# Performance work log

Measured on AMD Instinct MI355X. Metric: run time of the kernel, lower is better.

The kernel has to match this reference:

```python
import jax, jax.numpy as jnp
import numpy as np

N = 10000   # num nodes
E = 640000  # num edges
D_IN, D_HID, D_OUT = 128, 256, 128


def _cheb_layer(x, src, dst, dis, W0, W1, b):
    """PyG ChebConv with K=2, sym norm, lambda_max=2.0 (no edge weights):
    out = x @ W0 + (L_hat x) @ W1 + b, with L_hat = -D^{-1/2} A D^{-1/2}."""
    norm = -(dis[src] * dis[dst])                       # [E]
    msg = norm[:, None] * x[src]                        # [E, d]
    tx1 = jax.ops.segment_sum(msg, dst, num_segments=N)  # [N, d]
    return x @ W0 + tx1 @ W1 + b


def setup_inputs() -> dict:
    key = jax.random.key(0)
    ks = jax.random.split(key, 10)

    def glorot(k, fan_in, fan_out):
        s = jnp.sqrt(6.0 / (fan_in + fan_out))
        return jax.random.uniform(k, (fan_in, fan_out), jnp.float32, -s, s)

    x = jax.random.normal(ks[0], (N, D_IN), jnp.float32)
    edge_index = jax.random.randint(ks[1], (2, E), 0, N, jnp.int64)
    edge_type = jax.random.randint(ks[2], (E,), 0, 5, jnp.int64)
    return {
        "x": x,
        "edge_index": edge_index,
        "edge_type": edge_type,
        "W01": glorot(ks[3], D_IN, D_HID),
        "W11": glorot(ks[4], D_IN, D_HID),
        "b1": jnp.zeros((D_HID,), jnp.float32),
        "W02": glorot(ks[5], D_HID, D_HID),
        "W12": glorot(ks[6], D_HID, D_HID),
        "b2": jnp.zeros((D_HID,), jnp.float32),
        "W03": glorot(ks[7], D_HID, D_OUT),
        "W13": glorot(ks[8], D_HID, D_OUT),
        "b3": jnp.zeros((D_OUT,), jnp.float32),
    }


def reference(x, edge_index, edge_type, W01, W11, b1, W02, W12, b2, W03, W13, b3):
    # edge_type is unused by ChebConv (matches the original forward signature).
    src, dst = edge_index[0], edge_index[1]
    deg = jax.ops.segment_sum(jnp.ones((E,), x.dtype), src, num_segments=N)
    dis = jnp.where(deg > 0, jax.lax.rsqrt(jnp.maximum(deg, 1.0)), 0.0)
    # eval mode: dropout(p=0.4) is identity
    h = jax.nn.relu(_cheb_layer(x, src, dst, dis, W01, W11, b1))
    h = jax.nn.relu(_cheb_layer(h, src, dst, dis, W02, W12, b2))
    return _cheb_layer(h, src, dst, dis, W03, W13, b3)
```

## Files before the change

### kernel.cpp

```cpp
#include <hip/hip_runtime.h>

#define D_IN 128
#define D_HID 256
#define D_OUT 128
#define NBIN 10240
#define HB 128

typedef __attribute__((ext_vector_type(8))) unsigned short ushort8v;
typedef __attribute__((ext_vector_type(4))) unsigned short ushort4v;
typedef __attribute__((ext_vector_type(8))) short short8v;
typedef __attribute__((ext_vector_type(4))) float f32x4;

__device__ __forceinline__ unsigned short f2bf(float f) {
    unsigned u = __float_as_uint(f);
    unsigned r = (u + 0x7fffu + ((u >> 16) & 1u)) >> 16;
    return (unsigned short)r;
}
__device__ __forceinline__ float bf2f(unsigned short b) {
    return __uint_as_float((unsigned)b << 16);
}


__global__ __launch_bounds__(256) void k_hist(const int* __restrict__ src, const int* __restrict__ dst,
                                              unsigned short* __restrict__ psrc,
                                              unsigned short* __restrict__ pdst,
                                              int E, int EPB) {
    __shared__ int hs[NBIN];
    __shared__ int hd[NBIN];
    int b = blockIdx.x, t = threadIdx.x;
    for (int i = t; i < NBIN; i += 256) { hs[i] = 0; hd[i] = 0; }
    __syncthreads();
    int beg = b * EPB, end = beg + EPB; if (end > E) end = E;
    for (int e = beg + t; e < end; e += 256) {
        atomicAdd(&hs[src[e]], 1);
        atomicAdd(&hd[dst[e]], 1);
    }
    __syncthreads();
    for (int i = t; i < NBIN; i += 256) {
        psrc[(size_t)b * NBIN + i] = (unsigned short)hs[i];
        pdst[(size_t)b * NBIN + i] = (unsigned short)hd[i];
    }
}


__global__ __launch_bounds__(256) void k_colsum(const unsigned short* __restrict__ psrc,
                                                unsigned short* __restrict__ pdst,
                                                float* __restrict__ dis, int* __restrict__ cnt) {
    int bin = blockIdx.x * 256 + threadIdx.x;
    if (bin >= NBIN) return;
    int degs = 0;
    for (int b = 0; b < HB; ++b) degs += psrc[(size_t)b * NBIN + bin];
    int c = 0;
    for (int b = 0; b < HB; ++b) {
        int v = pdst[(size_t)b * NBIN + bin];
        pdst[(size_t)b * NBIN + bin] = (unsigned short)c;
        c += v;
    }
    dis[bin] = degs > 0 ? rsqrtf((float)degs) : 0.f;
    cnt[bin] = c;
}


__global__ void k_scan(const int* __restrict__ cnt, int* __restrict__ off, int n, int E) {
    __shared__ int sums[256];
    int t = threadIdx.x;
    int chunk = (n + 255) / 256;
    int beg = t * chunk;
    int end = beg + chunk; if (end > n) end = n;
    int s = 0;
    for (int i = beg; i < end; ++i) s += cnt[i];
    sums[t] = s;
    __syncthreads();
    if (t == 0) {
        int running = 0;
        for (int i = 0; i < 256; ++i) { int tmp = sums[i]; sums[i] = running; running += tmp; }
        off[n] = E;
    }
    __syncthreads();
    int pre = sums[t];
    for (int i = beg; i < end; ++i) { off[i] = pre; pre += cnt[i]; }
}


__global__ __launch_bounds__(256) void k_scatter2(const int* __restrict__ src, const int* __restrict__ dst,
                                                  const float* __restrict__ dis, const int* __restrict__ off,
                                                  const unsigned short* __restrict__ pfx,
                                                  int2* __restrict__ edges, int E, int EPB) {
    __shared__ int lcnt[NBIN];
    int b = blockIdx.x, t = threadIdx.x;
    for (int i = t; i < NBIN; i += 256) lcnt[i] = 0;
    __syncthreads();
    int beg = b * EPB, end = beg + EPB; if (end > E) end = E;
    const unsigned short* pf = pfx + (size_t)b * NBIN;
    for (int e = beg + t; e < end; e += 256) {
        int s = src[e], d = dst[e];
        int r = atomicAdd(&lcnt[d], 1);
        int pos = off[d] + (int)pf[d] + r;
        float nv = -(dis[s] * dis[d]);
        edges[pos] = make_int2(s, __float_as_int(nv));
    }
}


struct WtrArgs {
    const float* W[6];
    unsigned short* T[6];
    int K[6];
    int N[6];
    const float* xin;
    unsigned short* xout;
    int nElem;
};

__global__ __launch_bounds__(256) void k_wtr7(WtrArgs args) {
    __shared__ float tile[32][33];
    int z = blockIdx.z;
    if (z == 6) {
        int bid = blockIdx.y * 8 + blockIdx.x;
        int stride = 64 * 256 * 4;
        for (int i = (bid * 256 + threadIdx.x) * 4; i < args.nElem; i += stride) {
            float4 v = *reinterpret_cast<const float4*>(&args.xin[i]);
            ushort4v o;
            o[0] = f2bf(v.x); o[1] = f2bf(v.y); o[2] = f2bf(v.z); o[3] = f2bf(v.w);
            *reinterpret_cast<ushort4v*>(&args.xout[i]) = o;
        }
        return;
    }
    const float* W = args.W[z];
    unsigned short* Wt = args.T[z];
    int K = args.K[z], N = args.N[z];
    int k0 = blockIdx.x * 32, n0 = blockIdx.y * 32;
    if (k0 >= K || n0 >= N) return;
    int tx = threadIdx.x & 31, ty = threadIdx.x >> 5;
    for (int i = ty; i < 32; i += 8) tile[i][tx] = W[(size_t)(k0 + i) * N + n0 + tx];
    __syncthreads();
    for (int i = ty; i < 32; i += 8) Wt[(size_t)(n0 + i) * K + k0 + tx] = f2bf(tile[tx][i]);
}


template<int D, bool STBF, bool STF32, bool ADDB>
__global__ __launch_bounds__(256) void k_agg_bf(const int* __restrict__ off,
                                                const int2* __restrict__ edges,
                                                const unsigned short* __restrict__ xb,
                                                unsigned short* __restrict__ outb,
                                                float* __restrict__ outf,
                                                const float* __restrict__ base, int n) {
    const int CHUNK = 128;
    const int TPN = CHUNK / 8;
    const int NPB = 256 / TPN;
    int tid = threadIdx.x;
    int node = blockIdx.x * NPB + tid / TPN;
    if (node >= n) return;
    int cbase = blockIdx.y * CHUNK + (tid % TPN) * 8;
    int i = off[node], end = off[node + 1];
    float acc[8] = {};
    for (; i + 7 < end; i += 8) {
        int2 e[8];
        #pragma unroll
        for (int u = 0; u < 8; ++u) e[u] = edges[i + u];
        ushort8v v[8];
        #pragma unroll
        for (int u = 0; u < 8; ++u)
            v[u] = *reinterpret_cast<const ushort8v*>(&xb[(size_t)e[u].x * D + cbase]);
        #pragma unroll
        for (int u = 0; u < 8; ++u) {
            float nv = __int_as_float(e[u].y);
            #pragma unroll
            for (int j = 0; j < 8; ++j)
                acc[j] += nv * bf2f(v[u][j]);
        }
    }
    for (; i + 1 < end; i += 2) {
        int2 e0 = edges[i], e1 = edges[i + 1];
        ushort8v v0 = *reinterpret_cast<const ushort8v*>(&xb[(size_t)e0.x * D + cbase]);
        ushort8v v1 = *reinterpret_cast<const ushort8v*>(&xb[(size_t)e1.x * D + cbase]);
        float n0 = __int_as_float(e0.y), n1 = __int_as_float(e1.y);
        #pragma unroll
        for (int j = 0; j < 8; ++j)
            acc[j] += n0 * bf2f(v0[j]) + n1 * bf2f(v1[j]);
    }
    if (i < end) {
        int2 e0 = edges[i];
        float n0 = __int_as_float(e0.y);
        ushort8v v0 = *reinterpret_cast<const ushort8v*>(&xb[(size_t)e0.x * D + cbase]);
        #pragma unroll
        for (int j = 0; j < 8; ++j)
            acc[j] += n0 * bf2f(v0[j]);
    }
    if (ADDB) {
        float4 b0 = *reinterpret_cast<const float4*>(&base[(size_t)node * D + cbase]);
        float4 b1 = *reinterpret_cast<const float4*>(&base[(size_t)node * D + cbase + 4]);
        acc[0] += b0.x; acc[1] += b0.y; acc[2] += b0.z; acc[3] += b0.w;
        acc[4] += b1.x; acc[5] += b1.y; acc[6] += b1.z; acc[7] += b1.w;
    }
    if (STBF) {
        ushort8v ob;
        #pragma unroll
        for (int j = 0; j < 8; ++j) ob[j] = f2bf(acc[j]);
        *reinterpret_cast<ushort8v*>(&outb[(size_t)node * D + cbase]) = ob;
    }
    if (STF32) {
        float4 o0, o1;
        o0.x = acc[0]; o0.y = acc[1]; o0.z = acc[2]; o0.w = acc[3];
        o1.x = acc[4]; o1.y = acc[5]; o1.z = acc[6]; o1.w = acc[7];
        *reinterpret_cast<float4*>(&outf[(size_t)node * D + cbase]) = o0;
        *reinterpret_cast<float4*>(&outf[(size_t)node * D + cbase + 4]) = o1;
    }
}


#define LDT 72

template<int K, bool RELU, bool HAS_B2, bool HAS_BIAS, bool ST_BF, bool ST_F32>
__global__ __launch_bounds__(256) void k_gemm_mfma(
        const unsigned short* __restrict__ A1, const unsigned short* __restrict__ W0t,
        const unsigned short* __restrict__ A2, const unsigned short* __restrict__ W1t,
        const float* __restrict__ bias,
        float* __restrict__ C, unsigned short* __restrict__ Cb, int M, int N) {
    __shared__ unsigned short As[64 * LDT];
    __shared__ unsigned short Bs[128 * LDT];
    int tid = threadIdx.x, lane = tid & 63, wave = tid >> 6;
    int wm = wave >> 1, wn = wave & 1;
    int row0 = blockIdx.x * 64, col0 = blockIdx.y * 128;
    f32x4 acc[2][4];
    #pragma unroll
    for (int i = 0; i < 2; ++i)
        #pragma unroll
        for (int j = 0; j < 4; ++j)
            acc[i][j] = (f32x4){0.f, 0.f, 0.f, 0.f};

    int aRow = wm * 32 + (lane & 15);
    int bRow = wn * 64 + (lane & 15);
    int kOff = (lane >> 4) * 8;
    int sr = tid >> 2, sc = (tid & 3) * 8;
    int gra = row0 + sr; if (gra >= M) gra = M - 1;

    const int npass = HAS_B2 ? 2 : 1;
    for (int pass = 0; pass < npass; ++pass) {
        const unsigned short* A = pass ? A2 : A1;
        const unsigned short* W = pass ? W1t : W0t;
        for (int k0 = 0; k0 < K; k0 += 64) {
            #pragma unroll
            for (int h = 0; h < 2; ++h) {
                ushort8v va = *reinterpret_cast<const ushort8v*>(&A[(size_t)gra * K + k0 + sc + h * 32]);
                *reinterpret_cast<ushort8v*>(&As[sr * LDT + sc + h * 32]) = va;
            }
            #pragma unroll
            for (int g = 0; g < 2; ++g)
                #pragma unroll
                for (int h = 0; h < 2; ++h) {
                    int r = sr + g * 64;
                    ushort8v vb = *reinterpret_cast<const ushort8v*>(&W[(size_t)(col0 + r) * K + k0 + sc + h * 32]);
                    *reinterpret_cast<ushort8v*>(&Bs[r * LDT + sc + h * 32]) = vb;
                }
            __syncthreads();
            #pragma unroll
            for (int kk = 0; kk < 2; ++kk) {
                int ko = kOff + kk * 32;
                short8v a[2], bb[4];
                #pragma unroll
                for (int i = 0; i < 2; ++i)
                    a[i] = *reinterpret_cast<const short8v*>(&As[(aRow + i * 16) * LDT + ko]);
                #pragma unroll
                for (int i = 0; i < 4; ++i)
                    bb[i] = *reinterpret_cast<const short8v*>(&Bs[(bRow + i * 16) * LDT + ko]);
                #pragma unroll
                for (int mi = 0; mi < 2; ++mi)
                    #pragma unroll
                    for (int ni = 0; ni < 4; ++ni)
                        acc[mi][ni] = __builtin_amdgcn_mfma_f32_16x16x32_bf16(a[mi], bb[ni], acc[mi][ni], 0, 0, 0);
            }
            __syncthreads();
        }
    }

    int colBase = col0 + wn * 64 + (lane & 15);
    int rowSub = (lane >> 4) * 4;
    #pragma unroll
    for (int mi = 0; mi < 2; ++mi) {
        int rowF = row0 + wm * 32 + mi * 16 + rowSub;
        #pragma unroll
        for (int r = 0; r < 4; ++r) {
            int gr = rowF + r;
            if (gr < M) {
                #pragma unroll
                for (int ni = 0; ni < 4; ++ni) {
                    int gc = colBase + ni * 16;
                    float v = acc[mi][ni][r];
                    if (HAS_BIAS) v += bias[gc];
                    if (RELU)     v = fmaxf(v, 0.f);
                    if (ST_F32)   C[(size_t)gr * N + gc] = v;
                    if (ST_BF)    Cb[(size_t)gr * N + gc] = f2bf(v);
                }
            }
        }
    }
}


template<int K>
__global__ __launch_bounds__(256) void k_gemm_dual(
        const unsigned short* __restrict__ A1, const unsigned short* __restrict__ W03t,
        const unsigned short* __restrict__ W13t, const float* __restrict__ bias,
        float* __restrict__ part, unsigned short* __restrict__ y3b, int M) {
    const int N = 128;
    __shared__ unsigned short As[64 * LDT];
    __shared__ unsigned short Bs[128 * LDT];
    int tid = threadIdx.x, lane = tid & 63, wave = tid >> 6;
    int wm = wave >> 1, wn = wave & 1;
    int row0 = blockIdx.x * 64;
    const unsigned short* W = blockIdx.y ? W13t : W03t;
    f32x4 acc[2][4];
    #pragma unroll
    for (int i = 0; i < 2; ++i)
        #pragma unroll
        for (int j = 0; j < 4; ++j)
            acc[i][j] = (f32x4){0.f, 0.f, 0.f, 0.f};

    int aRow = wm * 32 + (lane & 15);
    int bRow = wn * 64 + (lane & 15);
    int kOff = (lane >> 4) * 8;
    int sr = tid >> 2, sc = (tid & 3) * 8;
    int gra = row0 + sr; if (gra >= M) gra = M - 1;

    for (int k0 = 0; k0 < K; k0 += 64) {
        #pragma unroll
        for (int h = 0; h < 2; ++h) {
            ushort8v va = *reinterpret_cast<const ushort8v*>(&A1[(size_t)gra * K + k0 + sc + h * 32]);
            *reinterpret_cast<ushort8v*>(&As[sr * LDT + sc + h * 32]) = va;
        }
        #pragma unroll
        for (int g = 0; g < 2; ++g)
            #pragma unroll
            for (int h = 0; h < 2; ++h) {
                int r = sr + g * 64;
                ushort8v vb = *reinterpret_cast<const ushort8v*>(&W[(size_t)r * K + k0 + sc + h * 32]);
                *reinterpret_cast<ushort8v*>(&Bs[r * LDT + sc + h * 32]) = vb;
            }
        __syncthreads();
        #pragma unroll
        for (int kk = 0; kk < 2; ++kk) {
            int ko = kOff + kk * 32;
            short8v a[2], bb[4];
            #pragma unroll
            for (int i = 0; i < 2; ++i)
                a[i] = *reinterpret_cast<const short8v*>(&As[(aRow + i * 16) * LDT + ko]);
            #pragma unroll
            for (int i = 0; i < 4; ++i)
                bb[i] = *reinterpret_cast<const short8v*>(&Bs[(bRow + i * 16) * LDT + ko]);
            #pragma unroll
            for (int mi = 0; mi < 2; ++mi)
                #pragma unroll
                for (int ni = 0; ni < 4; ++ni)
                    acc[mi][ni] = __builtin_amdgcn_mfma_f32_16x16x32_bf16(a[mi], bb[ni], acc[mi][ni], 0, 0, 0);
        }
        __syncthreads();
    }

    int colBase = wn * 64 + (lane & 15);
    int rowSub = (lane >> 4) * 4;
    bool isPart = (blockIdx.y == 0);
    #pragma unroll
    for (int mi = 0; mi < 2; ++mi) {
        int rowF = row0 + wm * 32 + mi * 16 + rowSub;
        #pragma unroll
        for (int r = 0; r < 4; ++r) {
            int gr = rowF + r;
            if (gr < M) {
                #pragma unroll
                for (int ni = 0; ni < 4; ++ni) {
                    int gc = colBase + ni * 16;
                    float v = acc[mi][ni][r];
                    if (isPart) part[(size_t)gr * N + gc] = v + bias[gc];
                    else        y3b[(size_t)gr * N + gc] = f2bf(v);
                }
            }
        }
    }
}


extern "C" void kernel_launch(void* const* d_in, const int* in_sizes, int n_in,
                              void* d_out, int out_size, void* d_ws, size_t ws_size,
                              hipStream_t stream) {
    const float* x   = (const float*)d_in[0];
    const int*   ei  = (const int*)d_in[1];
    const float* W01 = (const float*)d_in[3];
    const float* W11 = (const float*)d_in[4];
    const float* b1  = (const float*)d_in[5];
    const float* W02 = (const float*)d_in[6];
    const float* W12 = (const float*)d_in[7];
    const float* b2  = (const float*)d_in[8];
    const float* W03 = (const float*)d_in[9];
    const float* W13 = (const float*)d_in[10];
    const float* b3  = (const float*)d_in[11];
    float* out = (float*)d_out;

    const int n = in_sizes[0] / D_IN;
    const int E = in_sizes[1] / 2;
    const int* src = ei;
    const int* dst = ei + E;
    const int EPB = (E + HB - 1) / HB;

    char* wsb = (char*)d_ws;
    float* dis   = (float*)wsb;                   wsb += NBIN * 4;
    int*   cnt   = (int*)wsb;                     wsb += NBIN * 4;
    int*   off   = (int*)wsb;                     wsb += (NBIN + 16) * 4;
    unsigned short* psrc = (unsigned short*)wsb;  wsb += (size_t)HB * NBIN * 2;
    unsigned short* pdst = (unsigned short*)wsb;  wsb += (size_t)HB * NBIN * 2;
    int2*  edges = (int2*)wsb;                    wsb += (size_t)E * 8;
    unsigned short* txb  = (unsigned short*)wsb;  wsb += (size_t)n * D_HID * 2;
    float*          part = (float*)wsb;           wsb += (size_t)n * D_OUT * 4;
    unsigned short* x_bf = (unsigned short*)wsb;  wsb += (size_t)n * D_IN * 2;
    unsigned short* h1_bf = (unsigned short*)wsb; wsb += (size_t)n * D_HID * 2;
    unsigned short* h2_bf = (unsigned short*)wsb; wsb += (size_t)n * D_HID * 2;
    unsigned short* y3_bf = (unsigned short*)wsb; wsb += (size_t)n * D_OUT * 2;
    unsigned short* W01t = (unsigned short*)wsb;  wsb += (size_t)D_IN  * D_HID * 2;
    unsigned short* W11t = (unsigned short*)wsb;  wsb += (size_t)D_IN  * D_HID * 2;
    unsigned short* W02t = (unsigned short*)wsb;  wsb += (size_t)D_HID * D_HID * 2;
    unsigned short* W12t = (unsigned short*)wsb;  wsb += (size_t)D_HID * D_HID * 2;
    unsigned short* W03t = (unsigned short*)wsb;  wsb += (size_t)D_HID * D_OUT * 2;
    unsigned short* W13t = (unsigned short*)wsb;  wsb += (size_t)D_HID * D_OUT * 2;

    const int gmx = (n + 63) / 64;
    const int gax = (n + 15) / 16;

    k_hist<<<HB, 256, 0, stream>>>(src, dst, psrc, pdst, E, EPB);
    k_colsum<<<NBIN / 256, 256, 0, stream>>>(psrc, pdst, dis, cnt);
    k_scan<<<1, 256, 0, stream>>>(cnt, off, n, E);
    k_scatter2<<<HB, 256, 0, stream>>>(src, dst, dis, off, pdst, edges, E, EPB);

    {
        WtrArgs wa;
        wa.W[0] = W01; wa.T[0] = W01t; wa.K[0] = D_IN;  wa.N[0] = D_HID;
        wa.W[1] = W11; wa.T[1] = W11t; wa.K[1] = D_IN;  wa.N[1] = D_HID;
        wa.W[2] = W02; wa.T[2] = W02t; wa.K[2] = D_HID; wa.N[2] = D_HID;
        wa.W[3] = W12; wa.T[3] = W12t; wa.K[3] = D_HID; wa.N[3] = D_HID;
        wa.W[4] = W03; wa.T[4] = W03t; wa.K[4] = D_HID; wa.N[4] = D_OUT;
        wa.W[5] = W13; wa.T[5] = W13t; wa.K[5] = D_HID; wa.N[5] = D_OUT;
        wa.xin = x; wa.xout = x_bf; wa.nElem = n * D_IN;
        k_wtr7<<<dim3(8, 8, 7), 256, 0, stream>>>(wa);
    }

    k_agg_bf<D_IN, true, false, false><<<dim3(gax, 1), 256, 0, stream>>>(
        off, edges, x_bf, txb, nullptr, nullptr, n);
    k_gemm_mfma<D_IN, true, true, true, true, false><<<dim3(gmx, D_HID / 128), 256, 0, stream>>>(
        x_bf, W01t, txb, W11t, b1, nullptr, h1_bf, n, D_HID);

    k_agg_bf<D_HID, true, false, false><<<dim3(gax, 2), 256, 0, stream>>>(
        off, edges, h1_bf, txb, nullptr, nullptr, n);
    k_gemm_mfma<D_HID, true, true, true, true, false><<<dim3(gmx, D_HID / 128), 256, 0, stream>>>(
        h1_bf, W02t, txb, W12t, b2, nullptr, h2_bf, n, D_HID);

    k_gemm_dual<D_HID><<<dim3(gmx, 2), 256, 0, stream>>>(
        h2_bf, W03t, W13t, b3, part, y3_bf, n);
    k_agg_bf<D_OUT, false, true, true><<<dim3(gax, 1), 256, 0, stream>>>(
        off, edges, y3_bf, nullptr, out, part, n);
}
```

Measured before the change: 178.9 us.

## Pack CSR edges into 32-bit words and software-pipeline the aggregation gather

```diff
diff --git a/kernel.cpp b/kernel.cpp
--- a/kernel.cpp
+++ b/kernel.cpp
@@ -4,7 +4,7 @@
 #define D_HID 256
 #define D_OUT 128
 #define NBIN 10240
-#define HB 128
+#define HB 64
 
 typedef __attribute__((ext_vector_type(8))) unsigned short ushort8v;
 typedef __attribute__((ext_vector_type(4))) unsigned short ushort4v;
@@ -85,7 +85,7 @@
 __global__ __launch_bounds__(256) void k_scatter2(const int* __restrict__ src, const int* __restrict__ dst,
                                                   const float* __restrict__ dis, const int* __restrict__ off,
                                                   const unsigned short* __restrict__ pfx,
-                                                  int2* __restrict__ edges, int E, int EPB) {
+                                                  unsigned* __restrict__ edges, int E, int EPB) {
     __shared__ int lcnt[NBIN];
     int b = blockIdx.x, t = threadIdx.x;
     for (int i = t; i < NBIN; i += 256) lcnt[i] = 0;
@@ -97,7 +97,7 @@
         int r = atomicAdd(&lcnt[d], 1);
         int pos = off[d] + (int)pf[d] + r;
         float nv = -(dis[s] * dis[d]);
-        edges[pos] = make_int2(s, __float_as_int(nv));
+        edges[pos] = ((unsigned)s << 16) | (unsigned)f2bf(nv);
     }
 }
 
@@ -138,9 +138,23 @@
 }
 
 
+#define AGG_GATHER(eSet, vSet)                                                        \
+    _Pragma("unroll")                                                                 \
+    for (int u = 0; u < 8; ++u)                                                       \
+        vSet[u] = *reinterpret_cast<const ushort8v*>(&xb[(size_t)(eSet[u] >> 16) * D + cbase]);
+
+#define AGG_ACCUM(eSet, vSet)                                                         \
+    _Pragma("unroll")                                                                 \
+    for (int u = 0; u < 8; ++u) {                                                     \
+        float nv = __uint_as_float(eSet[u] << 16);                                    \
+        _Pragma("unroll")                                                             \
+        for (int j = 0; j < 8; ++j)                                                   \
+            acc[j] += nv * bf2f(vSet[u][j]);                                          \
+    }
+
 template<int D, bool STBF, bool STF32, bool ADDB>
 __global__ __launch_bounds__(256) void k_agg_bf(const int* __restrict__ off,
-                                                const int2* __restrict__ edges,
+                                                const unsigned* __restrict__ edges,
                                                 const unsigned short* __restrict__ xb,
                                                 unsigned short* __restrict__ outb,
                                                 float* __restrict__ outf,
@@ -154,39 +168,47 @@
     int cbase = blockIdx.y * CHUNK + (tid % TPN) * 8;
     int i = off[node], end = off[node + 1];
     float acc[8] = {};
-    for (; i + 7 < end; i += 8) {
-        int2 e[8];
-        #pragma unroll
-        for (int u = 0; u < 8; ++u) e[u] = edges[i + u];
-        ushort8v v[8];
-        #pragma unroll
-        for (int u = 0; u < 8; ++u)
-            v[u] = *reinterpret_cast<const ushort8v*>(&xb[(size_t)e[u].x * D + cbase]);
-        #pragma unroll
-        for (int u = 0; u < 8; ++u) {
-            float nv = __int_as_float(e[u].y);
-            #pragma unroll
-            for (int j = 0; j < 8; ++j)
-                acc[j] += nv * bf2f(v[u][j]);
-        }
-    }
-    for (; i + 1 < end; i += 2) {
-        int2 e0 = edges[i], e1 = edges[i + 1];
-        ushort8v v0 = *reinterpret_cast<const ushort8v*>(&xb[(size_t)e0.x * D + cbase]);
-        ushort8v v1 = *reinterpret_cast<const ushort8v*>(&xb[(size_t)e1.x * D + cbase]);
-        float n0 = __int_as_float(e0.y), n1 = __int_as_float(e1.y);
+    int nb = (end - i) >> 3;
+
+    if (nb > 0) {
+        unsigned e0[8], e1[8];
+        ushort8v v0[8], v1[8];
+        #pragma unroll
+        for (int u = 0; u < 8; ++u) e0[u] = edges[i + u];
+        AGG_GATHER(e0, v0)
+        int b = 1;
+        for (; b + 1 < nb; b += 2) {
+            int base1 = i + b * 8;
+            #pragma unroll
+            for (int u = 0; u < 8; ++u) e1[u] = edges[base1 + u];
+            AGG_GATHER(e1, v1)
+            AGG_ACCUM(e0, v0)
+            int base0 = i + (b + 1) * 8;
+            #pragma unroll
+            for (int u = 0; u < 8; ++u) e0[u] = edges[base0 + u];
+            AGG_GATHER(e0, v0)
+            AGG_ACCUM(e1, v1)
+        }
+        if (b < nb) {
+            int base1 = i + b * 8;
+            #pragma unroll
+            for (int u = 0; u < 8; ++u) e1[u] = edges[base1 + u];
+            AGG_GATHER(e1, v1)
+            AGG_ACCUM(e0, v0)
+            AGG_ACCUM(e1, v1)
+        } else {
+            AGG_ACCUM(e0, v0)
+        }
+    }
+    for (int t = i + nb * 8; t < end; ++t) {
+        unsigned e = edges[t];
+        float nv = __uint_as_float(e << 16);
+        ushort8v v = *reinterpret_cast<const ushort8v*>(&xb[(size_t)(e >> 16) * D + cbase]);
         #pragma unroll
         for (int j = 0; j < 8; ++j)
-            acc[j] += n0 * bf2f(v0[j]) + n1 * bf2f(v1[j]);
-    }
-    if (i < end) {
-        int2 e0 = edges[i];
-        float n0 = __int_as_float(e0.y);
-        ushort8v v0 = *reinterpret_cast<const ushort8v*>(&xb[(size_t)e0.x * D + cbase]);
-        #pragma unroll
-        for (int j = 0; j < 8; ++j)
-            acc[j] += n0 * bf2f(v0[j]);
-    }
+            acc[j] += nv * bf2f(v[j]);
+    }
+
     if (ADDB) {
         float4 b0 = *reinterpret_cast<const float4*>(&base[(size_t)node * D + cbase]);
         float4 b1 = *reinterpret_cast<const float4*>(&base[(size_t)node * D + cbase + 4]);
@@ -408,7 +430,7 @@
     int*   off   = (int*)wsb;                     wsb += (NBIN + 16) * 4;
     unsigned short* psrc = (unsigned short*)wsb;  wsb += (size_t)HB * NBIN * 2;
     unsigned short* pdst = (unsigned short*)wsb;  wsb += (size_t)HB * NBIN * 2;
-    int2*  edges = (int2*)wsb;                    wsb += (size_t)E * 8;
+    unsigned* edges = (unsigned*)wsb;             wsb += (size_t)E * 4;
     unsigned short* txb  = (unsigned short*)wsb;  wsb += (size_t)n * D_HID * 2;
     float*          part = (float*)wsb;           wsb += (size_t)n * D_OUT * 4;
     unsigned short* x_bf = (unsigned short*)wsb;  wsb += (size_t)n * D_IN * 2;
```

New measurement: 191.5 us. +7.1%, slower.
